# Optimization experiments

Hardware: AMD Instinct MI355X
Metric: run time of the kernel (lower is better)

## Reference

```python
import jax, jax.numpy as jnp
import numpy as np

B, T, K = 32, 64, 5
VOCAB, DE, DA, DI, H = 32000, 300, 300, 2048, 512


def setup_inputs() -> dict:
    key = jax.random.key(0)
    ks = jax.random.split(key, 8)
    return {
        'top_k_attributes': jax.random.randint(ks[0], (B, K), 0, 1000, dtype=jnp.int32),
        'mean_image_features': jax.random.normal(ks[1], (B, DI), jnp.float32),
        'seq_inputs': jax.random.randint(ks[2], (B, T), 0, VOCAB, dtype=jnp.int32),
        'lengths': jax.random.randint(ks[3], (B,), 1, T + 1, dtype=jnp.int32),
        'word_emb': jax.random.normal(ks[4], (VOCAB, DE), jnp.float32) * 0.02,
        'attr_emb': jax.random.normal(ks[5], (1000, DA), jnp.float32) * 0.02,
        'lstm_kernel': jax.random.normal(ks[6], (DE + DI + DA + H, 4 * H), jnp.float32) * 0.02,
        'lstm_bias': jnp.zeros((4 * H,), jnp.float32),
        'W_logits': jax.random.normal(ks[7], (H, VOCAB), jnp.float32) * 0.02,
        'b_logits': jnp.zeros((VOCAB,), jnp.float32),
    }


def reference(top_k_attributes, mean_image_features, seq_inputs, lengths,
              word_emb, attr_emb, lstm_kernel, lstm_bias, W_logits, b_logits):
    # attribute features: lookup + mean over the K attributes
    attr_feats = attr_emb[top_k_attributes]              # [B,K,DA]
    mean_attr = attr_feats.mean(axis=1)                  # [B,DA]
    feats = jnp.concatenate([mean_image_features, mean_attr], axis=-1)  # [B,DI+DA]

    x = word_emb[seq_inputs]                             # [B,T,DE]
    # per-step cell input = concat(word_emb_t, image+attr features)
    inp = jnp.concatenate([x, jnp.broadcast_to(feats[:, None, :], (B, T, feats.shape[-1]))], axis=-1)

    def step(carry, x_t):
        h, c = carry
        z = jnp.concatenate([x_t, h], axis=-1) @ lstm_kernel + lstm_bias  # [B,4H]
        i, f, g, o = jnp.split(z, 4, axis=-1)
        c = jax.nn.sigmoid(f) * c + jax.nn.sigmoid(i) * jnp.tanh(g)
        h = jax.nn.sigmoid(o) * jnp.tanh(c)
        return (h, c), h

    h0 = jnp.zeros((B, H), inp.dtype)
    (_, _), h_seq = jax.lax.scan(step, (h0, h0), jnp.transpose(inp, (1, 0, 2)))
    h_seq = jnp.transpose(h_seq, (1, 0, 2))              # [B,T,H]

    # dynamic_rnn zeros activations past each sequence length
    mask = (jnp.arange(T)[None, :] < lengths[:, None])[:, :, None]
    h_seq = jnp.where(mask, h_seq, 0.0)

    logits = jnp.einsum('bth,hv->btv', h_seq, W_logits) + b_logits  # [B,T,V]
    return logits, jnp.argmax(logits, axis=-1).astype(jnp.int32)
```

## Files before the change

kernel.cpp:

```cpp
#include <hip/hip_runtime.h>
#include <hip/hip_bf16.h>
#include <math.h>

#define BATCH 32
#define TSEQ  64
#define KATTR 5
#define VOCAB 32000
#define DE    300
#define DA    300
#define DI    2048
#define HDIM  512
#define G4    2048
#define WOFF  (DE + DI + DA)

__global__ void zero_kernel(float* __restrict__ p, int n) {
    int i = blockIdx.x * blockDim.x + threadIdx.x;
    if (i < n) p[i] = 0.f;
}

__device__ __forceinline__ unsigned int fkey(float f) {
    unsigned int u = __float_as_uint(f);
    return (u & 0x80000000u) ? ~u : (u | 0x80000000u);
}
__device__ __forceinline__ void amax_upd(unsigned int& bk, int& bi, float v, int idx) {
    unsigned int k = fkey(v);
    if (k > bk || (k == bk && idx < bi)) { bk = k; bi = idx; }
}

__global__ void mean_attr_kernel(const int* __restrict__ topk,
                                 const float* __restrict__ attr_emb,
                                 float* __restrict__ mean_attr) {
    int b = blockIdx.x;
    int tid = threadIdx.x;
    if (tid < DA) {
        float s = 0.f;
        #pragma unroll
        for (int q = 0; q < KATTR; ++q) {
            int a = topk[b * KATTR + q];
            s += attr_emb[(size_t)a * DA + tid];
        }
        mean_attr[b * DA + tid] = s / (float)KATTR;
    }
}

__launch_bounds__(256)
__global__ void zf_kernel(const float* __restrict__ img,
                          const float* __restrict__ mean_attr,
                          const float* __restrict__ Wk,
                          const float* __restrict__ bias,
                          float* __restrict__ zf) {
    int b = blockIdx.y;
    int j = blockIdx.x * 256 + threadIdx.x;
    float acc = bias[j];
    const float* wimg = Wk + (size_t)DE * G4 + j;
    const float* irow = img + b * DI;
    #pragma unroll 8
    for (int k = 0; k < DI; ++k) acc += irow[k] * wimg[(size_t)k * G4];
    const float* wattr = Wk + (size_t)(DE + DI) * G4 + j;
    const float* arow = mean_attr + b * DA;
    #pragma unroll 4
    for (int k = 0; k < DA; ++k) acc += arow[k] * wattr[(size_t)k * G4];
    zf[b * G4 + j] = acc;
}

__launch_bounds__(256)
__global__ void whr_kernel(const float* __restrict__ Wk, float* __restrict__ Whr) {
    const int bid = blockIdx.x;
    const int tid = threadIdx.x;
    for (int it = 0; it < 16; ++it) {
        int Q = it * 256 + tid;
        int k = Q >> 3, jj = Q & 7;
        int g = jj >> 1, p = jj & 1;
        Whr[(size_t)bid * 4096 + Q] = Wk[(size_t)(WOFF + k) * G4 + g * HDIM + bid * 2 + p];
    }
}

template<bool GATHER, bool PERROW>
__launch_bounds__(256)
__global__ void gemm_tile(const float* __restrict__ A,
                          const int* __restrict__ gidx,
                          const float* __restrict__ Bm,
                          const float* __restrict__ addv,
                          float* __restrict__ C,
                          int M, int N, int K, int lda) {
    __shared__ __align__(16) float As[16][68];
    __shared__ __align__(16) float Bs[16][68];
    const int tid = threadIdx.x;
    const int n0 = blockIdx.x * 64;
    const int m0 = blockIdx.y * 64;
    const int tx = tid & 15, ty = tid >> 4;
    const int ar  = tid >> 2;
    const int akq = (tid & 3) << 2;
    const int bkr = tid >> 4;
    const int bc  = (tid & 15) << 2;

    size_t arow;
    if (GATHER) arow = (size_t)gidx[m0 + ar] * (size_t)lda;
    else        arow = (size_t)(m0 + ar) * (size_t)lda;

    float a00=0,a01=0,a02=0,a03=0, a10=0,a11=0,a12=0,a13=0;
    float a20=0,a21=0,a22=0,a23=0, a30=0,a31=0,a32=0,a33=0;

    for (int k0 = 0; k0 < K; k0 += 16) {
        int ka = k0 + akq;
        float4 av;
        if (ka + 4 <= K) {
            av = *(const float4*)(A + arow + ka);
        } else {
            av.x = (ka + 0 < K) ? A[arow + ka + 0] : 0.f;
            av.y = (ka + 1 < K) ? A[arow + ka + 1] : 0.f;
            av.z = (ka + 2 < K) ? A[arow + ka + 2] : 0.f;
            av.w = (ka + 3 < K) ? A[arow + ka + 3] : 0.f;
        }
        As[akq + 0][ar] = av.x;
        As[akq + 1][ar] = av.y;
        As[akq + 2][ar] = av.z;
        As[akq + 3][ar] = av.w;

        int kb = k0 + bkr;
        float4 bv;
        if (kb < K) bv = *(const float4*)(Bm + (size_t)kb * N + n0 + bc);
        else { bv.x = bv.y = bv.z = bv.w = 0.f; }
        *(float4*)&Bs[bkr][bc] = bv;

        __syncthreads();
        #pragma unroll
        for (int kk = 0; kk < 16; ++kk) {
            const float4 a4 = *(const float4*)&As[kk][ty << 2];
            const float4 b4 = *(const float4*)&Bs[kk][tx << 2];
            a00 += a4.x * b4.x; a01 += a4.x * b4.y; a02 += a4.x * b4.z; a03 += a4.x * b4.w;
            a10 += a4.y * b4.x; a11 += a4.y * b4.y; a12 += a4.y * b4.z; a13 += a4.y * b4.w;
            a20 += a4.z * b4.x; a21 += a4.z * b4.y; a22 += a4.z * b4.z; a23 += a4.z * b4.w;
            a30 += a4.w * b4.x; a31 += a4.w * b4.y; a32 += a4.w * b4.z; a33 += a4.w * b4.w;
        }
        __syncthreads();
    }

    float accs[4][4] = {{a00,a01,a02,a03},{a10,a11,a12,a13},{a20,a21,a22,a23},{a30,a31,a32,a33}};
    const int n = n0 + (tx << 2);
    #pragma unroll
    for (int i = 0; i < 4; ++i) {
        int m = m0 + (ty << 2) + i;
        const float* av2 = PERROW ? (addv + (size_t)(m >> 6) * N) : addv;
        float4 o;
        o.x = accs[i][0] + av2[n + 0];
        o.y = accs[i][1] + av2[n + 1];
        o.z = accs[i][2] + av2[n + 2];
        o.w = accs[i][3] + av2[n + 3];
        *(float4*)(C + (size_t)m * N + n) = o;
    }
}

__global__ void build_rows(const int* __restrict__ lengths,
                           int* __restrict__ rowlist, int* __restrict__ mact) {
    __shared__ int len[BATCH];
    __shared__ int off[BATCH + 1];
    int tid = threadIdx.x;
    if (tid < BATCH) len[tid] = lengths[tid];
    __syncthreads();
    if (tid == 0) {
        int s = 0;
        for (int b = 0; b < BATCH; ++b) { off[b] = s; s += len[b]; }
        off[BATCH] = s;
        *mact = s;
    }
    __syncthreads();
    int total = off[BATCH];
    for (int i = tid; i < BATCH * TSEQ; i += 256) {
        int b = i >> 6, t = i & 63;
        if (t < len[b]) rowlist[off[b] + t] = i;
    }
    for (int i = tid; i < BATCH * TSEQ; i += 256) {
        if (i >= total) rowlist[i] = 0;
    }
}

__launch_bounds__(256, 1)
__global__ void lstm_step2(const float* __restrict__ z_pre,
                           const float* __restrict__ Whr,
                           const float* __restrict__ hin,
                           float* __restrict__ hout,
                           float* __restrict__ cbuf,
                           float* __restrict__ h_seq,
                           const int* __restrict__ lengths,
                           int t) {
    __shared__ __align__(16) float hsT[HDIM][36];
    __shared__ __align__(16) float wsm[HDIM][12];
    __shared__ __align__(16) float zp[16 * 260];
    __shared__ float zfull[BATCH][8];
    const int bid = blockIdx.x;
    const int tid = threadIdx.x;

    float zp4[4] = {0, 0, 0, 0};
    int glen = 0, gb = 0, gkk = 0;
    float c_old = 0.f;
    if (tid < 64) {
        gb = tid & 31;
        int kp = tid >> 5;
        gkk = bid * 2 + kp;
        glen = lengths[gb];
        const float* zr = z_pre + ((size_t)(gb * TSEQ + t)) * G4 + gkk;
        zp4[0] = zr[0 * HDIM];
        zp4[1] = zr[1 * HDIM];
        zp4[2] = zr[2 * HDIM];
        zp4[3] = zr[3 * HDIM];
        c_old = cbuf[gkk * BATCH + gb];
    }

    #pragma unroll
    for (int it = 0; it < 16; ++it) {
        int Q = it * 256 + tid;
        int k = Q >> 3, bq = Q & 7;
        float4 v = *(const float4*)(hin + (size_t)Q * 4);
        *(float4*)&hsT[k][bq * 4] = v;
    }
    const float* wsrc = Whr + (size_t)bid * 4096;
    #pragma unroll
    for (int it = 0; it < 4; ++it) {
        int Q = it * 256 + tid;
        int k = Q >> 1, jjq = Q & 1;
        float4 v = *(const float4*)(wsrc + (size_t)Q * 4);
        *(float4*)&wsm[k][jjq * 4] = v;
    }
    __syncthreads();

    {
        const int kseg = tid >> 4;
        const int tile = tid & 15;
        const int b0 = (tile >> 1) << 2;
        const int j0 = (tile & 1) << 2;
        const int kb = kseg << 5;
        float a00=0,a01=0,a02=0,a03=0, a10=0,a11=0,a12=0,a13=0;
        float a20=0,a21=0,a22=0,a23=0, a30=0,a31=0,a32=0,a33=0;
        #pragma unroll 8
        for (int kk = 0; kk < 32; ++kk) {
            const int k = kb + kk;
            const float4 h4 = *(const float4*)&hsT[k][b0];
            const float4 w4 = *(const float4*)&wsm[k][j0];
            a00 += h4.x * w4.x; a01 += h4.x * w4.y; a02 += h4.x * w4.z; a03 += h4.x * w4.w;
            a10 += h4.y * w4.x; a11 += h4.y * w4.y; a12 += h4.y * w4.z; a13 += h4.y * w4.w;
            a20 += h4.z * w4.x; a21 += h4.z * w4.y; a22 += h4.z * w4.z; a23 += h4.z * w4.w;
            a30 += h4.w * w4.x; a31 += h4.w * w4.y; a32 += h4.w * w4.z; a33 += h4.w * w4.w;
        }
        float* zpr = &zp[kseg * 260 + tile * 16];
        *(float4*)(zpr + 0)  = make_float4(a00, a01, a02, a03);
        *(float4*)(zpr + 4)  = make_float4(a10, a11, a12, a13);
        *(float4*)(zpr + 8)  = make_float4(a20, a21, a22, a23);
        *(float4*)(zpr + 12) = make_float4(a30, a31, a32, a33);
    }
    __syncthreads();

    {
        const int b = tid & 31, jj = tid >> 5;
        const int tile2 = ((b >> 2) << 1) + (jj >> 2);
        const int e = ((b & 3) << 2) + (jj & 3);
        float s = 0.f;
        #pragma unroll
        for (int ks = 0; ks < 16; ++ks) s += zp[ks * 260 + tile2 * 16 + e];
        zfull[b][jj] = s;
    }
    __syncthreads();

    if (tid < 64) {
        const int kp = tid >> 5;
        float zi = zfull[gb][0 * 2 + kp] + zp4[0];
        float zF = zfull[gb][1 * 2 + kp] + zp4[1];
        float zg = zfull[gb][2 * 2 + kp] + zp4[2];
        float zo = zfull[gb][3 * 2 + kp] + zp4[3];
        float si = 1.f / (1.f + expf(-zi));
        float sf = 1.f / (1.f + expf(-zF));
        float so = 1.f / (1.f + expf(-zo));
        float c_new = sf * c_old + si * tanhf(zg);
        float h_new = so * tanhf(c_new);
        cbuf[gkk * BATCH + gb] = c_new;
        hout[gkk * BATCH + gb] = h_new;
        h_seq[((size_t)(gb * TSEQ + t)) * HDIM + gkk] = (t < glen) ? h_new : 0.f;
    }
}

__launch_bounds__(256)
__global__ void fill_masked(const int* __restrict__ lengths,
                            const float* __restrict__ blog,
                            float* __restrict__ logits) {
    int row = blockIdx.x;
    int b = row >> 6, t = row & 63;
    if (t < lengths[b]) return;
    float* p = logits + (size_t)row * VOCAB;
    for (int v = threadIdx.x * 4; v < VOCAB; v += 256 * 4) {
        float4 o;
        o.x = blog[v + 0]; o.y = blog[v + 1]; o.z = blog[v + 2]; o.w = blog[v + 3];
        *(float4*)(p + v) = o;
    }
}

__launch_bounds__(256)
__global__ void gemm_logits128(const float* __restrict__ A,
                               const int* __restrict__ rowlist,
                               const int* __restrict__ mactp,
                               const float* __restrict__ Bm,
                               const float* __restrict__ blog,
                               float* __restrict__ C,
                               unsigned long long* __restrict__ packed) {
    const int Mact = *mactp;
    const int chunk = gridDim.x >> 3;
    const int L = (blockIdx.x & 7) * chunk + (blockIdx.x >> 3);
    const int m0 = (L & 15) * 128;
    const int n0 = (L >> 4) * 128;
    if (m0 >= Mact) return;

    __shared__ __align__(16) float As[16][132];
    __shared__ __align__(16) float Bs[16][132];
    const int tid = threadIdx.x;
    const int tx = tid & 15, ty = tid >> 4;

    const int am  = tid >> 2;
    const int akq = (tid & 3) << 2;
    const size_t arow0 = (size_t)rowlist[m0 + am]      * HDIM;
    const size_t arow1 = (size_t)rowlist[m0 + 64 + am] * HDIM;
    const int bk = tid >> 5;
    const int bc = (tid & 31) << 2;

    float c00[4][4] = {}, c01[4][4] = {}, c10[4][4] = {}, c11[4][4] = {};

    for (int k0 = 0; k0 < HDIM; k0 += 16) {
        const float4 av0 = *(const float4*)(A + arow0 + k0 + akq);
        const float4 av1 = *(const float4*)(A + arow1 + k0 + akq);
        As[akq + 0][am] = av0.x;
        As[akq + 1][am] = av0.y;
        As[akq + 2][am] = av0.z;
        As[akq + 3][am] = av0.w;
        As[akq + 0][64 + am] = av1.x;
        As[akq + 1][64 + am] = av1.y;
        As[akq + 2][64 + am] = av1.z;
        As[akq + 3][64 + am] = av1.w;
        const float4 bv0 = *(const float4*)(Bm + (size_t)(k0 + bk)     * VOCAB + n0 + bc);
        const float4 bv1 = *(const float4*)(Bm + (size_t)(k0 + 8 + bk) * VOCAB + n0 + bc);
        *(float4*)&Bs[bk][bc]     = bv0;
        *(float4*)&Bs[bk + 8][bc] = bv1;
        __syncthreads();
        #pragma unroll
        for (int kk = 0; kk < 16; ++kk) {
            const float4 aL = *(const float4*)&As[kk][ty << 2];
            const float4 aH = *(const float4*)&As[kk][64 + (ty << 2)];
            const float4 bL = *(const float4*)&Bs[kk][tx << 2];
            const float4 bH = *(const float4*)&Bs[kk][64 + (tx << 2)];
            const float a_[8] = {aL.x, aL.y, aL.z, aL.w, aH.x, aH.y, aH.z, aH.w};
            const float b_[8] = {bL.x, bL.y, bL.z, bL.w, bH.x, bH.y, bH.z, bH.w};
            #pragma unroll
            for (int i = 0; i < 4; ++i) {
                #pragma unroll
                for (int j = 0; j < 4; ++j) {
                    c00[i][j] += a_[i]     * b_[j];
                    c01[i][j] += a_[i]     * b_[4 + j];
                    c10[i][j] += a_[4 + i] * b_[j];
                    c11[i][j] += a_[4 + i] * b_[4 + j];
                }
            }
        }
        __syncthreads();
    }

    const int nL = n0 + (tx << 2);
    const int nH = nL + 64;
    const float4 gL = *(const float4*)(blog + nL);
    const float4 gH = *(const float4*)(blog + nH);
    const float gLa[4] = {gL.x, gL.y, gL.z, gL.w};
    const float gHa[4] = {gH.x, gH.y, gH.z, gH.w};
    #pragma unroll
    for (int i = 0; i < 4; ++i) {
        const int mL = m0 + (ty << 2) + i;
        if (mL < Mact) {
            const int rid = rowlist[mL];
            const size_t rm = (size_t)rid * VOCAB;
            float4 oL, oH;
            oL.x = c00[i][0] + gLa[0]; oL.y = c00[i][1] + gLa[1];
            oL.z = c00[i][2] + gLa[2]; oL.w = c00[i][3] + gLa[3];
            oH.x = c01[i][0] + gHa[0]; oH.y = c01[i][1] + gHa[1];
            oH.z = c01[i][2] + gHa[2]; oH.w = c01[i][3] + gHa[3];
            *(float4*)(C + rm + nL) = oL;
            *(float4*)(C + rm + nH) = oH;
            unsigned int bkk = 0u; int bii = 0x7FFFFFFF;
            amax_upd(bkk, bii, oL.x, nL + 0); amax_upd(bkk, bii, oL.y, nL + 1);
            amax_upd(bkk, bii, oL.z, nL + 2); amax_upd(bkk, bii, oL.w, nL + 3);
            amax_upd(bkk, bii, oH.x, nH + 0); amax_upd(bkk, bii, oH.y, nH + 1);
            amax_upd(bkk, bii, oH.z, nH + 2); amax_upd(bkk, bii, oH.w, nH + 3);
            unsigned long long pv = ((unsigned long long)bkk << 32) | (unsigned int)(~bii);
            #pragma unroll
            for (int off = 8; off > 0; off >>= 1) {
                unsigned int hi = (unsigned int)(pv >> 32), lo = (unsigned int)pv;
                unsigned int ohi = __shfl_xor(hi, off, 16);
                unsigned int olo = __shfl_xor(lo, off, 16);
                unsigned long long ov = ((unsigned long long)ohi << 32) | olo;
                if (ov > pv) pv = ov;
            }
            if (tx == 0) atomicMax(&packed[rid], pv);
        }
        const int mH = mL + 64;
        if (mH < Mact) {
            const int rid = rowlist[mH];
            const size_t rm = (size_t)rid * VOCAB;
            float4 oL, oH;
            oL.x = c10[i][0] + gLa[0]; oL.y = c10[i][1] + gLa[1];
            oL.z = c10[i][2] + gLa[2]; oL.w = c10[i][3] + gLa[3];
            oH.x = c11[i][0] + gHa[0]; oH.y = c11[i][1] + gHa[1];
            oH.z = c11[i][2] + gHa[2]; oH.w = c11[i][3] + gHa[3];
            *(float4*)(C + rm + nL) = oL;
            *(float4*)(C + rm + nH) = oH;
            unsigned int bkk = 0u; int bii = 0x7FFFFFFF;
            amax_upd(bkk, bii, oL.x, nL + 0); amax_upd(bkk, bii, oL.y, nL + 1);
            amax_upd(bkk, bii, oL.z, nL + 2); amax_upd(bkk, bii, oL.w, nL + 3);
            amax_upd(bkk, bii, oH.x, nH + 0); amax_upd(bkk, bii, oH.y, nH + 1);
            amax_upd(bkk, bii, oH.z, nH + 2); amax_upd(bkk, bii, oH.w, nH + 3);
            unsigned long long pv = ((unsigned long long)bkk << 32) | (unsigned int)(~bii);
            #pragma unroll
            for (int off = 8; off > 0; off >>= 1) {
                unsigned int hi = (unsigned int)(pv >> 32), lo = (unsigned int)pv;
                unsigned int ohi = __shfl_xor(hi, off, 16);
                unsigned int olo = __shfl_xor(lo, off, 16);
                unsigned long long ov = ((unsigned long long)ohi << 32) | olo;
                if (ov > pv) pv = ov;
            }
            if (tx == 0) atomicMax(&packed[rid], pv);
        }
    }
}

__launch_bounds__(256)
__global__ void finalize_argmax(const unsigned long long* __restrict__ packed,
                                const float* __restrict__ blog,
                                const int* __restrict__ lengths,
                                float* __restrict__ outa) {
    __shared__ unsigned long long red[256];
    __shared__ int slen[BATCH];
    const int tid = threadIdx.x;
    unsigned int bk = 0u; int bi = 0x7FFFFFFF;
    for (int v = tid; v < VOCAB; v += 256) {
        amax_upd(bk, bi, blog[v], v);
    }
    red[tid] = ((unsigned long long)bk << 32) | (unsigned int)(~bi);
    if (tid < BATCH) slen[tid] = lengths[tid];
    __syncthreads();
    for (int s = 128; s > 0; s >>= 1) {
        if (tid < s) { if (red[tid + s] > red[tid]) red[tid] = red[tid + s]; }
        __syncthreads();
    }
    const int bias_idx = (int)(~(unsigned int)(red[0] & 0xFFFFFFFFull));
    for (int row = tid; row < BATCH * TSEQ; row += 256) {
        int b = row >> 6, t = row & 63;
        int idx = (t < slen[b]) ? (int)(~(unsigned int)(packed[row] & 0xFFFFFFFFull))
                                : bias_idx;
        outa[row] = (float)idx;
    }
}

extern "C" void kernel_launch(void* const* d_in, const int* in_sizes, int n_in,
                              void* d_out, int out_size, void* d_ws, size_t ws_size,
                              hipStream_t stream) {
    const int*   topk     = (const int*)d_in[0];
    const float* img      = (const float*)d_in[1];
    const int*   seq      = (const int*)d_in[2];
    const int*   lengths  = (const int*)d_in[3];
    const float* word_emb = (const float*)d_in[4];
    const float* attr_emb = (const float*)d_in[5];
    const float* Wk       = (const float*)d_in[6];
    const float* bias     = (const float*)d_in[7];
    const float* Wlog     = (const float*)d_in[8];
    const float* blog     = (const float*)d_in[9];

    float* out_logits = (float*)d_out;
    float* out_argmax = out_logits + (size_t)BATCH * TSEQ * VOCAB;

    float* ws        = (float*)d_ws;
    float* mean_attr = ws;
    float* zf        = mean_attr + BATCH * DA;
    float* cbuf      = zf + BATCH * G4;
    float* hb0       = cbuf + HDIM * BATCH;
    float* hb1       = hb0 + HDIM * BATCH;
    float* h_seq     = hb1 + HDIM * BATCH;
    float* Whr       = h_seq + (size_t)BATCH * TSEQ * HDIM;
    int*   rowlist   = (int*)(Whr + (size_t)256 * 4096);
    int*   mact      = rowlist + BATCH * TSEQ;
    unsigned long long* packed = (unsigned long long*)(mact + 2);
    float* z_pre     = out_logits;

    zero_kernel<<<dim3((2 * HDIM * BATCH + 255) / 256), 256, 0, stream>>>(cbuf, 2 * HDIM * BATCH);
    zero_kernel<<<dim3(16), 256, 0, stream>>>((float*)packed, 4096);

    build_rows<<<1, 256, 0, stream>>>(lengths, rowlist, mact);

    whr_kernel<<<dim3(256), 256, 0, stream>>>(Wk, Whr);

    mean_attr_kernel<<<dim3(BATCH), 320, 0, stream>>>(topk, attr_emb, mean_attr);

    zf_kernel<<<dim3(G4 / 256, BATCH), 256, 0, stream>>>(img, mean_attr, Wk, bias, zf);

    gemm_tile<true, true><<<dim3(G4 / 64, (BATCH * TSEQ) / 64), 256, 0, stream>>>(
        word_emb, seq, Wk, zf, z_pre, BATCH * TSEQ, G4, DE, DE);

    float* hin = hb0;
    float* hout = hb1;
    for (int t = 0; t < TSEQ; ++t) {
        lstm_step2<<<dim3(256), 256, 0, stream>>>(z_pre, Whr, hin, hout, cbuf, h_seq, lengths, t);
        float* tmp = hin; hin = hout; hout = tmp;
    }

    fill_masked<<<dim3(BATCH * TSEQ), 256, 0, stream>>>(lengths, blog, out_logits);

    gemm_logits128<<<dim3((VOCAB / 128) * ((BATCH * TSEQ) / 128)), 256, 0, stream>>>(
        h_seq, rowlist, mact, Wlog, blog, out_logits, packed);

    finalize_argmax<<<dim3(1), 256, 0, stream>>>(packed, blog, lengths, out_argmax);
}
```

Measured before the change: 1.382 ms.

## Double K tile and register-prefetch next tile in logits GEMM

The logits GEMM now stages 32-deep K slices in shared memory instead of 16, which halves the number of barrier pairs per output tile. The next slice's global loads go into registers before the inner FMA loop runs, so memory latency overlaps with compute. In exchange, shared memory use doubles and register pressure rises from the 8 extra float4 prefetch registers, which may lower occupancy.

```diff
diff --git a/kernel.cpp b/kernel.cpp
--- a/kernel.cpp
+++ b/kernel.cpp
@@ -308,38 +308,50 @@
     const int n0 = (L >> 4) * 128;
     if (m0 >= Mact) return;
 
-    __shared__ __align__(16) float As[16][132];
-    __shared__ __align__(16) float Bs[16][132];
+    __shared__ __align__(16) float As[32][132];
+    __shared__ __align__(16) float Bs[32][132];
     const int tid = threadIdx.x;
     const int tx = tid & 15, ty = tid >> 4;
 
-    const int am  = tid >> 2;
-    const int akq = (tid & 3) << 2;
-    const size_t arow0 = (size_t)rowlist[m0 + am]      * HDIM;
-    const size_t arow1 = (size_t)rowlist[m0 + 64 + am] * HDIM;
-    const int bk = tid >> 5;
+    const int ar4 = tid >> 3;
+    const int ak  = (tid & 7) << 2;
+    size_t arows[4];
+    #pragma unroll
+    for (int i = 0; i < 4; ++i)
+        arows[i] = (size_t)rowlist[m0 + ar4 + 32 * i] * HDIM;
+    const int kr = tid >> 5;
     const int bc = (tid & 31) << 2;
 
     float c00[4][4] = {}, c01[4][4] = {}, c10[4][4] = {}, c11[4][4] = {};
 
-    for (int k0 = 0; k0 < HDIM; k0 += 16) {
-        const float4 av0 = *(const float4*)(A + arow0 + k0 + akq);
-        const float4 av1 = *(const float4*)(A + arow1 + k0 + akq);
-        As[akq + 0][am] = av0.x;
-        As[akq + 1][am] = av0.y;
-        As[akq + 2][am] = av0.z;
-        As[akq + 3][am] = av0.w;
-        As[akq + 0][64 + am] = av1.x;
-        As[akq + 1][64 + am] = av1.y;
-        As[akq + 2][64 + am] = av1.z;
-        As[akq + 3][64 + am] = av1.w;
-        const float4 bv0 = *(const float4*)(Bm + (size_t)(k0 + bk)     * VOCAB + n0 + bc);
-        const float4 bv1 = *(const float4*)(Bm + (size_t)(k0 + 8 + bk) * VOCAB + n0 + bc);
-        *(float4*)&Bs[bk][bc]     = bv0;
-        *(float4*)&Bs[bk + 8][bc] = bv1;
+    float4 av[4], bv[4];
+    #pragma unroll
+    for (int i = 0; i < 4; ++i) {
+        av[i] = *(const float4*)(A + arows[i] + ak);
+        bv[i] = *(const float4*)(Bm + (size_t)(kr + 8 * i) * VOCAB + n0 + bc);
+    }
+
+    for (int k0 = 0; k0 < HDIM; k0 += 32) {
+        #pragma unroll
+        for (int i = 0; i < 4; ++i) {
+            As[ak + 0][ar4 + 32 * i] = av[i].x;
+            As[ak + 1][ar4 + 32 * i] = av[i].y;
+            As[ak + 2][ar4 + 32 * i] = av[i].z;
+            As[ak + 3][ar4 + 32 * i] = av[i].w;
+            *(float4*)&Bs[kr + 8 * i][bc] = bv[i];
+        }
         __syncthreads();
+
+        if (k0 + 32 < HDIM) {
+            #pragma unroll
+            for (int i = 0; i < 4; ++i) {
+                av[i] = *(const float4*)(A + arows[i] + k0 + 32 + ak);
+                bv[i] = *(const float4*)(Bm + (size_t)(k0 + 32 + kr + 8 * i) * VOCAB + n0 + bc);
+            }
+        }
+
         #pragma unroll
-        for (int kk = 0; kk < 16; ++kk) {
+        for (int kk = 0; kk < 32; ++kk) {
             const float4 aL = *(const float4*)&As[kk][ty << 2];
             const float4 aH = *(const float4*)&As[kk][64 + (ty << 2)];
             const float4 bL = *(const float4*)&Bs[kk][tx << 2];
```

Measured after the change: 1.416 ms. 2.5% more time.

## Fuse LSTM timesteps into one persistent cooperative kernel with grid barrier

Applied to the files above, without the earlier changes.

Replaces 64 per-timestep kernel launches with one cooperative kernel that loops over time. Recurrent weights stay in shared memory across steps and the cell state stays in registers. Steps are separated by a hierarchical atomic grid barrier, and h is exchanged through relaxed agent-scope atomics. This removes per-launch overhead and the repeated weight reloads, but risks barrier latency and memory-ordering problems, and the spin loop has a timeout that could silently break synchronisation.

```diff
diff --git a/kernel.cpp b/kernel.cpp
--- a/kernel.cpp
+++ b/kernel.cpp
@@ -175,15 +175,35 @@
     }
 }
 
+__device__ __forceinline__ void gridbar2(int* __restrict__ bar, int t, int bid) {
+    __syncthreads();
+    if (threadIdx.x == 0) {
+        asm volatile("s_waitcnt vmcnt(0)" ::: "memory");
+        const int g = bid >> 3;
+        int old = __hip_atomic_fetch_add(&bar[g * 32], 1, __ATOMIC_RELAXED, __HIP_MEMORY_SCOPE_AGENT);
+        if (old == t * 8 + 7) {
+            int ro = __hip_atomic_fetch_add(&bar[2048], 1, __ATOMIC_RELAXED, __HIP_MEMORY_SCOPE_AGENT);
+            if (ro == t * 32 + 31) {
+                __hip_atomic_store(&bar[2080], t + 1, __ATOMIC_RELAXED, __HIP_MEMORY_SCOPE_AGENT);
+            }
+        }
+        int spins = 0;
+        while (__hip_atomic_load(&bar[2080], __ATOMIC_RELAXED, __HIP_MEMORY_SCOPE_AGENT) <= t
+               && ++spins < 100000) {
+            __builtin_amdgcn_s_sleep(2);
+        }
+    }
+    __syncthreads();
+}
+
 __launch_bounds__(256, 1)
-__global__ void lstm_step2(const float* __restrict__ z_pre,
-                           const float* __restrict__ Whr,
-                           const float* __restrict__ hin,
-                           float* __restrict__ hout,
-                           float* __restrict__ cbuf,
-                           float* __restrict__ h_seq,
-                           const int* __restrict__ lengths,
-                           int t) {
+__global__ void lstm_scan(const float* __restrict__ z_pre,
+                          const float* __restrict__ Whr,
+                          float* __restrict__ hb0,
+                          float* __restrict__ hb1,
+                          float* __restrict__ h_seq,
+                          const int* __restrict__ lengths,
+                          int* __restrict__ bar) {
     __shared__ __align__(16) float hsT[HDIM][36];
     __shared__ __align__(16) float wsm[HDIM][12];
     __shared__ __align__(16) float zp[16 * 260];
@@ -191,29 +211,6 @@
     const int bid = blockIdx.x;
     const int tid = threadIdx.x;
 
-    float zp4[4] = {0, 0, 0, 0};
-    int glen = 0, gb = 0, gkk = 0;
-    float c_old = 0.f;
-    if (tid < 64) {
-        gb = tid & 31;
-        int kp = tid >> 5;
-        gkk = bid * 2 + kp;
-        glen = lengths[gb];
-        const float* zr = z_pre + ((size_t)(gb * TSEQ + t)) * G4 + gkk;
-        zp4[0] = zr[0 * HDIM];
-        zp4[1] = zr[1 * HDIM];
-        zp4[2] = zr[2 * HDIM];
-        zp4[3] = zr[3 * HDIM];
-        c_old = cbuf[gkk * BATCH + gb];
-    }
-
-    #pragma unroll
-    for (int it = 0; it < 16; ++it) {
-        int Q = it * 256 + tid;
-        int k = Q >> 3, bq = Q & 7;
-        float4 v = *(const float4*)(hin + (size_t)Q * 4);
-        *(float4*)&hsT[k][bq * 4] = v;
-    }
     const float* wsrc = Whr + (size_t)bid * 4096;
     #pragma unroll
     for (int it = 0; it < 4; ++it) {
@@ -222,59 +219,102 @@
         float4 v = *(const float4*)(wsrc + (size_t)Q * 4);
         *(float4*)&wsm[k][jjq * 4] = v;
     }
-    __syncthreads();
-
-    {
-        const int kseg = tid >> 4;
-        const int tile = tid & 15;
-        const int b0 = (tile >> 1) << 2;
-        const int j0 = (tile & 1) << 2;
-        const int kb = kseg << 5;
-        float a00=0,a01=0,a02=0,a03=0, a10=0,a11=0,a12=0,a13=0;
-        float a20=0,a21=0,a22=0,a23=0, a30=0,a31=0,a32=0,a33=0;
-        #pragma unroll 8
-        for (int kk = 0; kk < 32; ++kk) {
-            const int k = kb + kk;
-            const float4 h4 = *(const float4*)&hsT[k][b0];
-            const float4 w4 = *(const float4*)&wsm[k][j0];
-            a00 += h4.x * w4.x; a01 += h4.x * w4.y; a02 += h4.x * w4.z; a03 += h4.x * w4.w;
-            a10 += h4.y * w4.x; a11 += h4.y * w4.y; a12 += h4.y * w4.z; a13 += h4.y * w4.w;
-            a20 += h4.z * w4.x; a21 += h4.z * w4.y; a22 += h4.z * w4.z; a23 += h4.z * w4.w;
-            a30 += h4.w * w4.x; a31 += h4.w * w4.y; a32 += h4.w * w4.z; a33 += h4.w * w4.w;
-        }
-        float* zpr = &zp[kseg * 260 + tile * 16];
-        *(float4*)(zpr + 0)  = make_float4(a00, a01, a02, a03);
-        *(float4*)(zpr + 4)  = make_float4(a10, a11, a12, a13);
-        *(float4*)(zpr + 8)  = make_float4(a20, a21, a22, a23);
-        *(float4*)(zpr + 12) = make_float4(a30, a31, a32, a33);
-    }
-    __syncthreads();
-
-    {
-        const int b = tid & 31, jj = tid >> 5;
-        const int tile2 = ((b >> 2) << 1) + (jj >> 2);
-        const int e = ((b & 3) << 2) + (jj & 3);
-        float s = 0.f;
-        #pragma unroll
-        for (int ks = 0; ks < 16; ++ks) s += zp[ks * 260 + tile2 * 16 + e];
-        zfull[b][jj] = s;
-    }
-    __syncthreads();
-
+
+    int glen = 0, gb = 0, gkk = 0;
+    float c_reg = 0.f;
+    const float* zr = nullptr;
     if (tid < 64) {
-        const int kp = tid >> 5;
-        float zi = zfull[gb][0 * 2 + kp] + zp4[0];
-        float zF = zfull[gb][1 * 2 + kp] + zp4[1];
-        float zg = zfull[gb][2 * 2 + kp] + zp4[2];
-        float zo = zfull[gb][3 * 2 + kp] + zp4[3];
-        float si = 1.f / (1.f + expf(-zi));
-        float sf = 1.f / (1.f + expf(-zF));
-        float so = 1.f / (1.f + expf(-zo));
-        float c_new = sf * c_old + si * tanhf(zg);
-        float h_new = so * tanhf(c_new);
-        cbuf[gkk * BATCH + gb] = c_new;
-        hout[gkk * BATCH + gb] = h_new;
-        h_seq[((size_t)(gb * TSEQ + t)) * HDIM + gkk] = (t < glen) ? h_new : 0.f;
+        gb = tid & 31;
+        int kp = tid >> 5;
+        gkk = bid * 2 + kp;
+        glen = lengths[gb];
+        zr = z_pre + ((size_t)(gb * TSEQ)) * G4 + gkk;
+    }
+
+    const int kseg = tid >> 4;
+    const int tile = tid & 15;
+    const int b0 = (tile >> 1) << 2;
+    const int j0 = (tile & 1) << 2;
+    const int kb = kseg << 5;
+    const int rb = tid & 31, rjj = tid >> 5;
+    const int tile2 = ((rb >> 2) << 1) + (rjj >> 2);
+    const int e = ((rb & 3) << 2) + (rjj & 3);
+
+    for (int t = 0; t < TSEQ; ++t) {
+        const float* hin  = (t & 1) ? hb1 : hb0;
+        float*       hout = (t & 1) ? hb0 : hb1;
+
+        float zp4[4] = {0, 0, 0, 0};
+        if (tid < 64) {
+            const float* z = zr + (size_t)t * G4;
+            zp4[0] = z[0 * HDIM];
+            zp4[1] = z[1 * HDIM];
+            zp4[2] = z[2 * HDIM];
+            zp4[3] = z[3 * HDIM];
+        }
+
+        {
+            const unsigned long long* h8 = (const unsigned long long*)hin;
+            #pragma unroll
+            for (int it = 0; it < 32; ++it) {
+                int P = it * 256 + tid;
+                unsigned long long v = __hip_atomic_load(&h8[P], __ATOMIC_RELAXED,
+                                                         __HIP_MEMORY_SCOPE_AGENT);
+                int k = P >> 4;
+                int b = (P & 15) << 1;
+                float2 f;
+                f.x = __uint_as_float((unsigned int)(v & 0xFFFFFFFFull));
+                f.y = __uint_as_float((unsigned int)(v >> 32));
+                *(float2*)&hsT[k][b] = f;
+            }
+        }
+        __syncthreads();
+
+        {
+            float a00=0,a01=0,a02=0,a03=0, a10=0,a11=0,a12=0,a13=0;
+            float a20=0,a21=0,a22=0,a23=0, a30=0,a31=0,a32=0,a33=0;
+            #pragma unroll 8
+            for (int kk = 0; kk < 32; ++kk) {
+                const int k = kb + kk;
+                const float4 h4 = *(const float4*)&hsT[k][b0];
+                const float4 w4 = *(const float4*)&wsm[k][j0];
+                a00 += h4.x * w4.x; a01 += h4.x * w4.y; a02 += h4.x * w4.z; a03 += h4.x * w4.w;
+                a10 += h4.y * w4.x; a11 += h4.y * w4.y; a12 += h4.y * w4.z; a13 += h4.y * w4.w;
+                a20 += h4.z * w4.x; a21 += h4.z * w4.y; a22 += h4.z * w4.z; a23 += h4.z * w4.w;
+                a30 += h4.w * w4.x; a31 += h4.w * w4.y; a32 += h4.w * w4.z; a33 += h4.w * w4.w;
+            }
+            float* zpr = &zp[kseg * 260 + tile * 16];
+            *(float4*)(zpr + 0)  = make_float4(a00, a01, a02, a03);
+            *(float4*)(zpr + 4)  = make_float4(a10, a11, a12, a13);
+            *(float4*)(zpr + 8)  = make_float4(a20, a21, a22, a23);
+            *(float4*)(zpr + 12) = make_float4(a30, a31, a32, a33);
+        }
+        __syncthreads();
+
+        {
+            float s = 0.f;
+            #pragma unroll
+            for (int ks = 0; ks < 16; ++ks) s += zp[ks * 260 + tile2 * 16 + e];
+            zfull[rb][rjj] = s;
+        }
+        __syncthreads();
+
+        if (tid < 64) {
+            float zi = zfull[gb][0 * 2 + (tid >> 5)] + zp4[0];
+            float zF = zfull[gb][1 * 2 + (tid >> 5)] + zp4[1];
+            float zg = zfull[gb][2 * 2 + (tid >> 5)] + zp4[2];
+            float zo = zfull[gb][3 * 2 + (tid >> 5)] + zp4[3];
+            float si = 1.f / (1.f + expf(-zi));
+            float sf = 1.f / (1.f + expf(-zF));
+            float so = 1.f / (1.f + expf(-zo));
+            float c_new = sf * c_reg + si * tanhf(zg);
+            float h_new = so * tanhf(c_new);
+            c_reg = c_new;
+            __hip_atomic_store(&hout[gkk * BATCH + gb], h_new,
+                               __ATOMIC_RELAXED, __HIP_MEMORY_SCOPE_AGENT);
+            h_seq[((size_t)(gb * TSEQ + t)) * HDIM + gkk] = (t < glen) ? h_new : 0.f;
+        }
+        if (t != TSEQ - 1) gridbar2(bar, t, bid);
     }
 }
 
@@ -481,9 +521,11 @@
     int*   rowlist   = (int*)(Whr + (size_t)256 * 4096);
     int*   mact      = rowlist + BATCH * TSEQ;
     unsigned long long* packed = (unsigned long long*)(mact + 2);
+    int*   bar       = (int*)cbuf;
     float* z_pre     = out_logits;
 
-    zero_kernel<<<dim3((2 * HDIM * BATCH + 255) / 256), 256, 0, stream>>>(cbuf, 2 * HDIM * BATCH);
+    zero_kernel<<<dim3((2 * HDIM * BATCH + 255) / 256), 256, 0, stream>>>(hb0, 2 * HDIM * BATCH);
+    zero_kernel<<<dim3(16), 256, 0, stream>>>((float*)bar, 4096);
     zero_kernel<<<dim3(16), 256, 0, stream>>>((float*)packed, 4096);
 
     build_rows<<<1, 256, 0, stream>>>(lengths, rowlist, mact);
@@ -497,11 +539,11 @@
     gemm_tile<true, true><<<dim3(G4 / 64, (BATCH * TSEQ) / 64), 256, 0, stream>>>(
         word_emb, seq, Wk, zf, z_pre, BATCH * TSEQ, G4, DE, DE);
 
-    float* hin = hb0;
-    float* hout = hb1;
-    for (int t = 0; t < TSEQ; ++t) {
-        lstm_step2<<<dim3(256), 256, 0, stream>>>(z_pre, Whr, hin, hout, cbuf, h_seq, lengths, t);
-        float* tmp = hin; hin = hout; hout = tmp;
+    {
+        void* kargs[] = {(void*)&z_pre, (void*)&Whr, (void*)&hb0, (void*)&hb1,
+                         (void*)&h_seq, (void*)&lengths, (void*)&bar};
+        hipLaunchCooperativeKernel((const void*)lstm_scan, dim3(256), dim3(256),
+                                   kargs, 0, stream);
     }
 
     fill_masked<<<dim3(BATCH * TSEQ), 256, 0, stream>>>(lengths, blog, out_logits);
```

Result: slower. 1.844 ms (+33.4%).
